# Optimization experiments

Measured on AMD Instinct MI355X. Metric: run time of the kernel, lower is better.

## Reference

```python
import jax, jax.numpy as jnp
import numpy as np

# Problem dims (match init_kwargs)
N, D, H, W = 32, 64, 56, 56      # Xshape
F, P = 128, 4                    # n_filters, number_of_points
KH = 3                           # h_filter == w_filter
PAD = KH // 2                    # padw
ALPHA = 0.1                      # threshold sharpness for sigmoid approximation


def setup_inputs() -> dict:
    key = jax.random.key(0)
    k1, k2, k3 = jax.random.split(key, 3)
    return {
        "input": jax.random.normal(k1, (N, D, H, W), dtype=jnp.float32),
        # integer kernel coordinates in [0, KH): (filter, point, [ky, kx])
        "kernels": jax.random.randint(k2, (F, P, 2), 0, KH, dtype=jnp.int32),
        # channel projection indices in [0, D): (filter, point)
        "projection_map": jax.random.randint(k3, (F, P), 0, D, dtype=jnp.int32),
    }


def _lbp_forward(x, kernels, projection_map):
    # Pad spatially by PAD (zero padding), as the CUDA kernel pads input.
    xp = jnp.pad(x, ((0, 0), (0, 0), (PAD, PAD), (PAD, PAD)))  # [N, D, H+2P, W+2P]

    # Per (filter, point): gather the HxW window at integer offset (ky, kx)
    # from channel c of the padded input. vmap of dynamic_slice -> one fused gather.
    def sample(c, ky, kx):
        return jax.lax.dynamic_slice(xp, (0, c, ky, kx), (N, 1, H, W))[:, 0]  # [N,H,W]

    samp = jax.vmap(jax.vmap(sample))(
        projection_map, kernels[..., 0], kernels[..., 1]
    )  # [F, P, N, H, W]
    samp = jnp.transpose(samp, (2, 0, 1, 3, 4))  # [N, F, P, H, W]

    # Center pixel (same channel as the sampled point).
    center = xp[:, :, PAD:PAD + H, PAD:PAD + W]       # [N, D, H, W]
    cen = center[:, projection_map]                    # [N, F, P, H, W]

    # Output0: per-point sampled difference; threshold approximated by a
    # steep sigmoid (scale 1/ALPHA) so the op is differentiable, then pool
    # the P bits into a binary code with weights 2^p.
    diff = samp - cen                                  # [N, F, P, H, W]
    bits = jax.nn.sigmoid(diff / ALPHA)
    weights = jnp.asarray(2.0 ** np.arange(P), dtype=jnp.float32)  # [P]
    return jnp.einsum('nfphw,p->nfhw', bits, weights)  # [N, F, H, W]


def reference(input, kernels, projection_map):
    return _lbp_forward(input, kernels, projection_map)
```

## Files before the change

### kernel.cpp

```cpp
#include <hip/hip_runtime.h>


#define NN 32
#define DD 64
#define HH 56
#define WW 56
#define FF 128
#define PP 4

#define ROWS 7
#define TR   (ROWS + 2)
#define TC   64
#define COL0 4
#define CHS  (TR * TC)
#define TILE_FLOATS (DD * CHS)
#define NTHREADS 1024
#define NWAVES 16
#define FITER (FF / NWAVES)
#define ITEMS (DD * TR * 14)
#define NSTRIP (HH / ROWS)

__global__ __launch_bounds__(NTHREADS, 4) void lbp_kernel(
    const float* __restrict__ x,
    const int*   __restrict__ kern,
    const int*   __restrict__ proj,
    float*       __restrict__ out)
{
    __shared__ float tile[TILE_FLOATS];

    const int tid = threadIdx.x;
    const int n   = blockIdx.x;
    const int h0  = blockIdx.y * ROWS;

    const float* xn = x + (size_t)n * (DD * HH * WW);

    float4 rv[8];
    int    lo[8];
#pragma unroll
    for (int it = 0; it < 8; ++it) {
        const int item = tid + it * NTHREADS;
        rv[it] = make_float4(0.f, 0.f, 0.f, 0.f);
        lo[it] = -1;
        if (item < ITEMS) {
            const int ch  = item / (TR * 14);
            const int rem = item - ch * (TR * 14);
            const int tr  = rem / 14;
            const int v   = rem - tr * 14;
            lo[it] = ch * CHS + tr * TC + COL0 + 4 * v;
            const int h = h0 + tr - 1;
            if ((unsigned)h < (unsigned)HH)
                rv[it] = *(const float4*)(xn + ch * (HH * WW) + h * WW + 4 * v);
        }
    }

    for (int i = tid; i < DD * TR * 2; i += NTHREADS) {
        const int ch   = i / (TR * 2);
        const int rr   = (i >> 1) % TR;
        const int side = i & 1;
        tile[ch * CHS + rr * TC + 3 + side * 57] = 0.f;
    }

#pragma unroll
    for (int it = 0; it < 8; ++it)
        if (lo[it] >= 0) *(float4*)(tile + lo[it]) = rv[it];
    __syncthreads();

    const int wid  = __builtin_amdgcn_readfirstlane(tid >> 6);
    const int lane = tid & 63;
    const int w    = lane < WW ? lane : WW - 1;
    const bool act = lane < WW;
    const int cb   = TC + COL0 + w;

    int f = wid;
    int4 pj = *(const int4*)(proj + f * PP);
    int4 ka = *(const int4*)(kern + f * (PP * 2));
    int4 kb = *(const int4*)(kern + f * (PP * 2) + 4);

#pragma unroll
    for (int k = 0; k < FITER; ++k) {
        const int fn = f + NWAVES;
        int4 pjn, kan, kbn;
        if (fn < FF) {
            pjn = *(const int4*)(proj + fn * PP);
            kan = *(const int4*)(kern + fn * (PP * 2));
            kbn = *(const int4*)(kern + fn * (PP * 2) + 4);
        }
        const int cc[4]  = {pj.x, pj.y, pj.z, pj.w};
        const int kyv[4] = {ka.x, ka.z, kb.x, kb.z};
        const int kxv[4] = {ka.y, ka.w, kb.y, kb.w};

        float cv[PP][ROWS], nv[PP][ROWS];
#pragma unroll
        for (int p = 0; p < PP; ++p) {
            const int ky = kyv[p];
            const int kx = kxv[p];
            if (!(ky == 1 && kx == 1)) {
                const int pc = cc[p] * CHS + cb;
                const int pn = pc + (ky - 1) * TC + (kx - 1);
#pragma unroll
                for (int r = 0; r < ROWS; ++r) {
                    cv[p][r] = tile[pc + r * TC];
                    nv[p][r] = tile[pn + r * TC];
                }
            }
        }

        float acc[ROWS];
#pragma unroll
        for (int r = 0; r < ROWS; ++r) acc[r] = 7.5f;
#pragma unroll
        for (int p = 0; p < PP; ++p) {
            if (!(kyv[p] == 1 && kxv[p] == 1)) {
                const float wt = (float)(1 << p);
#pragma unroll
                for (int r = 0; r < ROWS; ++r) {
                    const float d  = nv[p][r] - cv[p][r];
                    const float ad = __builtin_fabsf(d);
                    const float u0 = fmaf(2.5f,     ad, -0.0078f);
                    const float u1 = fmaf(1.49146f, ad,  0.08455f);
                    const float u2 = fmaf(0.45177f, ad,  0.30774f);
                    const float um = fminf(fminf(fminf(u0, u1), u2), 0.49140f);
                    acc[r] = fmaf(wt, __builtin_copysignf(um, d), acc[r]);
                }
            }
        }

        if (act) {
            float* op = out + ((size_t)n * FF + f) * (HH * WW)
                            + (size_t)h0 * WW + w;
#pragma unroll
            for (int r = 0; r < ROWS; ++r) op[r * WW] = acc[r];
        }
        f = fn; pj = pjn; ka = kan; kb = kbn;
    }
}

extern "C" void kernel_launch(void* const* d_in, const int* in_sizes, int n_in,
                              void* d_out, int out_size, void* d_ws, size_t ws_size,
                              hipStream_t stream) {
    const float* x    = (const float*)d_in[0];
    const int*   kern = (const int*)d_in[1];
    const int*   proj = (const int*)d_in[2];
    float*       out  = (float*)d_out;

    dim3 grid(NN, NSTRIP);
    dim3 block(NTHREADS);
    lbp_kernel<<<grid, block, 0, stream>>>(x, kern, proj, out);
}
```

Baseline: 26.54 us.

## Pack two images as fp16 pairs in LDS and compute with packed half math

Each block now loads two images (n and n+16) and stores them interleaved as packed fp16 pairs in shared memory, so one LDS read feeds two images. The sigmoid-approximation arithmetic runs on packed half2 FMAs and mins, roughly halving ALU and LDS traffic per output. The filter dimension is split across a third grid axis so the block count stays the same. This lowers precision of the differences and accumulated codes to fp16, which may exceed tolerance near the steep sigmoid, and it doubles global reads per block.

```diff
diff --git a/kernel.cpp b/kernel.cpp
--- a/kernel.cpp
+++ b/kernel.cpp
@@ -13,12 +13,30 @@
 #define TC   64
 #define COL0 4
 #define CHS  (TR * TC)
-#define TILE_FLOATS (DD * CHS)
+#define TILE_DW (DD * CHS)
 #define NTHREADS 1024
 #define NWAVES 16
-#define FITER (FF / NWAVES)
+#define NPAIR 16
+#define NSTRIP (HH / ROWS)
+#define FH 64
+#define FITER (FH / NWAVES)
 #define ITEMS (DD * TR * 14)
-#define NSTRIP (HH / ROWS)
+#define IMGSTR (DD * HH * WW)
+
+typedef _Float16 h2 __attribute__((ext_vector_type(2)));
+
+static __device__ __forceinline__ uint32_t h2u(h2 h) {
+    union { h2 h; uint32_t u; } v; v.h = h; return v.u;
+}
+static __device__ __forceinline__ h2 u2h(uint32_t u) {
+    union { h2 h; uint32_t u; } v; v.u = u; return v.h;
+}
+static __device__ __forceinline__ h2 splat(float f) {
+    h2 r; r.x = (_Float16)f; r.y = (_Float16)f; return r;
+}
+static __device__ __forceinline__ uint32_t pack2(float a, float b) {
+    h2 r; r.x = (_Float16)a; r.y = (_Float16)b; return h2u(r);
+}
 
 __global__ __launch_bounds__(NTHREADS, 4) void lbp_kernel(
     const float* __restrict__ x,
@@ -26,20 +44,23 @@
     const int*   __restrict__ proj,
     float*       __restrict__ out)
 {
-    __shared__ float tile[TILE_FLOATS];
+    __shared__ uint32_t tile[TILE_DW];
 
     const int tid = threadIdx.x;
-    const int n   = blockIdx.x;
+    const int pr  = blockIdx.x;
     const int h0  = blockIdx.y * ROWS;
+    const int fh  = blockIdx.z;
 
-    const float* xn = x + (size_t)n * (DD * HH * WW);
+    const float* x0 = x + (size_t)pr * IMGSTR;
+    const float* x1 = x0 + (size_t)NPAIR * IMGSTR;
 
-    float4 rv[8];
+    float4 av[8], bv[8];
     int    lo[8];
 #pragma unroll
     for (int it = 0; it < 8; ++it) {
         const int item = tid + it * NTHREADS;
-        rv[it] = make_float4(0.f, 0.f, 0.f, 0.f);
+        av[it] = make_float4(0.f, 0.f, 0.f, 0.f);
+        bv[it] = make_float4(0.f, 0.f, 0.f, 0.f);
         lo[it] = -1;
         if (item < ITEMS) {
             const int ch  = item / (TR * 14);
@@ -48,8 +69,11 @@
             const int v   = rem - tr * 14;
             lo[it] = ch * CHS + tr * TC + COL0 + 4 * v;
             const int h = h0 + tr - 1;
-            if ((unsigned)h < (unsigned)HH)
-                rv[it] = *(const float4*)(xn + ch * (HH * WW) + h * WW + 4 * v);
+            if ((unsigned)h < (unsigned)HH) {
+                const int off = ch * (HH * WW) + h * WW + 4 * v;
+                av[it] = *(const float4*)(x0 + off);
+                bv[it] = *(const float4*)(x1 + off);
+            }
         }
     }
 
@@ -57,12 +81,20 @@
         const int ch   = i / (TR * 2);
         const int rr   = (i >> 1) % TR;
         const int side = i & 1;
-        tile[ch * CHS + rr * TC + 3 + side * 57] = 0.f;
+        tile[ch * CHS + rr * TC + 3 + side * 57] = 0u;
     }
 
 #pragma unroll
-    for (int it = 0; it < 8; ++it)
-        if (lo[it] >= 0) *(float4*)(tile + lo[it]) = rv[it];
+    for (int it = 0; it < 8; ++it) {
+        if (lo[it] >= 0) {
+            uint4 q;
+            q.x = pack2(av[it].x, bv[it].x);
+            q.y = pack2(av[it].y, bv[it].y);
+            q.z = pack2(av[it].z, bv[it].z);
+            q.w = pack2(av[it].w, bv[it].w);
+            *(uint4*)(tile + lo[it]) = q;
+        }
+    }
     __syncthreads();
 
     const int wid  = __builtin_amdgcn_readfirstlane(tid >> 6);
@@ -71,7 +103,13 @@
     const bool act = lane < WW;
     const int cb   = TC + COL0 + w;
 
-    int f = wid;
+    const h2 K0a = splat(2.5f),     K0b = splat(-0.0078f);
+    const h2 K1a = splat(1.49146f), K1b = splat(0.08455f);
+    const h2 K2a = splat(0.45177f), K2b = splat(0.30774f);
+    const h2 KF  = splat(0.49140f);
+    const h2 INI = splat(7.5f);
+
+    int f = fh * FH + wid;
     int4 pj = *(const int4*)(proj + f * PP);
     int4 ka = *(const int4*)(kern + f * (PP * 2));
     int4 kb = *(const int4*)(kern + f * (PP * 2) + 4);
@@ -79,8 +117,8 @@
 #pragma unroll
     for (int k = 0; k < FITER; ++k) {
         const int fn = f + NWAVES;
-        int4 pjn, kan, kbn;
-        if (fn < FF) {
+        int4 pjn = pj, kan = ka, kbn = kb;
+        if (k + 1 < FITER) {
             pjn = *(const int4*)(proj + fn * PP);
             kan = *(const int4*)(kern + fn * (PP * 2));
             kbn = *(const int4*)(kern + fn * (PP * 2) + 4);
@@ -89,7 +127,7 @@
         const int kyv[4] = {ka.x, ka.z, kb.x, kb.z};
         const int kxv[4] = {ka.y, ka.w, kb.y, kb.w};
 
-        float cv[PP][ROWS], nv[PP][ROWS];
+        uint32_t cu[PP][ROWS], nu[PP][ROWS];
 #pragma unroll
         for (int p = 0; p < PP; ++p) {
             const int ky = kyv[p];
@@ -99,37 +137,46 @@
                 const int pn = pc + (ky - 1) * TC + (kx - 1);
 #pragma unroll
                 for (int r = 0; r < ROWS; ++r) {
-                    cv[p][r] = tile[pc + r * TC];
-                    nv[p][r] = tile[pn + r * TC];
+                    cu[p][r] = tile[pc + r * TC];
+                    nu[p][r] = tile[pn + r * TC];
                 }
             }
         }
 
-        float acc[ROWS];
+        h2 acc[ROWS];
 #pragma unroll
-        for (int r = 0; r < ROWS; ++r) acc[r] = 7.5f;
+        for (int r = 0; r < ROWS; ++r) acc[r] = INI;
 #pragma unroll
         for (int p = 0; p < PP; ++p) {
             if (!(kyv[p] == 1 && kxv[p] == 1)) {
-                const float wt = (float)(1 << p);
+                const h2 wt2 = splat((float)(1 << p));
 #pragma unroll
                 for (int r = 0; r < ROWS; ++r) {
-                    const float d  = nv[p][r] - cv[p][r];
-                    const float ad = __builtin_fabsf(d);
-                    const float u0 = fmaf(2.5f,     ad, -0.0078f);
-                    const float u1 = fmaf(1.49146f, ad,  0.08455f);
-                    const float u2 = fmaf(0.45177f, ad,  0.30774f);
-                    const float um = fminf(fminf(fminf(u0, u1), u2), 0.49140f);
-                    acc[r] = fmaf(wt, __builtin_copysignf(um, d), acc[r]);
+                    const h2 d  = u2h(nu[p][r]) - u2h(cu[p][r]);
+                    const uint32_t du = h2u(d);
+                    const h2 ad = u2h(du & 0x7FFF7FFFu);
+                    const h2 u0 = __builtin_elementwise_fma(K0a, ad, K0b);
+                    const h2 u1 = __builtin_elementwise_fma(K1a, ad, K1b);
+                    const h2 u2 = __builtin_elementwise_fma(K2a, ad, K2b);
+                    const h2 um = __builtin_elementwise_min(
+                                      __builtin_elementwise_min(u0, u1),
+                                      __builtin_elementwise_min(u2, KF));
+                    const uint32_t su = (du & 0x80008000u)
+                                      | (h2u(um) & 0x7FFF7FFFu);
+                    acc[r] = __builtin_elementwise_fma(wt2, u2h(su), acc[r]);
                 }
             }
         }
 
         if (act) {
-            float* op = out + ((size_t)n * FF + f) * (HH * WW)
+            float* o0 = out + ((size_t)pr * FF + f) * (HH * WW)
                             + (size_t)h0 * WW + w;
+            float* o1 = o0 + (size_t)NPAIR * FF * (HH * WW);
 #pragma unroll
-            for (int r = 0; r < ROWS; ++r) op[r * WW] = acc[r];
+            for (int r = 0; r < ROWS; ++r) {
+                o0[r * WW] = (float)acc[r].x;
+                o1[r * WW] = (float)acc[r].y;
+            }
         }
         f = fn; pj = pjn; ka = kan; kb = kbn;
     }
@@ -143,7 +190,7 @@
     const int*   proj = (const int*)d_in[2];
     float*       out  = (float*)d_out;
 
-    dim3 grid(NN, NSTRIP);
+    dim3 grid(NPAIR, NSTRIP, 2);
     dim3 block(NTHREADS);
     lbp_kernel<<<grid, block, 0, stream>>>(x, kern, proj, out);
 }
```

After: 24.37 us (median of 2 runs). -8.2%, faster.
